# Kernel tuning notes

Measured on AMD Instinct MI355X. Metric: run time of the kernel, lower is better.

The kernel has to match this reference:

```python
import jax, jax.numpy as jnp
import numpy as np

B, C, H, W = 2, 128, 64, 64
EPS = 1e-5


def setup_inputs() -> dict:
    key = jax.random.key(0)
    ks = jax.random.split(key, 8)
    sc = 1.0 / np.sqrt(C)
    inp = {
        "x": jax.random.normal(ks[0], (B, C, H, W, 2), jnp.float32),
        # naive complex BN affine params: per-channel, per-component (real/imag)
        "bn_w": jnp.ones((C, 2), jnp.float32),
        "bn_b": jnp.zeros((C, 2), jnp.float32),
        # complex 1x1 conv weights: (out_c, in_c, 2) -> [..,0]=W_real, [..,1]=W_imag
        "wq": jax.random.normal(ks[1], (C, C, 2), jnp.float32) * sc,
        "bq": jnp.zeros((C, 2), jnp.float32),
        "wk": jax.random.normal(ks[2], (C, C, 2), jnp.float32) * sc,
        "bk": jnp.zeros((C, 2), jnp.float32),
        "wv": jax.random.normal(ks[3], (C, C, 2), jnp.float32) * sc,
        "bv": jnp.zeros((C, 2), jnp.float32),
        "gamma": jnp.float32(0.05),
    }
    return inp


def _complex_bn(x, w, b):
    # naive complex BN: normalize real and imag independently per channel
    # x: (B,C,H,W,2); stats over (B,H,W) per (C, component)
    mean = x.mean(axis=(0, 2, 3), keepdims=True)
    var = x.var(axis=(0, 2, 3), keepdims=True)
    xn = (x - mean) * jax.lax.rsqrt(var + EPS)
    return xn * w[None, :, None, None, :] + b[None, :, None, None, :]


def _complex_conv1x1(x, w, b):
    # x: (B,C,H,W,2); w: (O,C,2); b: (O,2)
    xr, xi = x[..., 0], x[..., 1]
    wr, wi = w[..., 0], w[..., 1]
    yr = jnp.einsum('oc,bchw->bohw', wr, xr) - jnp.einsum('oc,bchw->bohw', wi, xi)
    yi = jnp.einsum('oc,bchw->bohw', wr, xi) + jnp.einsum('oc,bchw->bohw', wi, xr)
    yr = yr + b[:, 0][None, :, None, None]
    yi = yi + b[:, 1][None, :, None, None]
    return jnp.stack([yr, yi], axis=-1)


def _attention(x, wq, bq, wk, bk, wv, bv, gamma):
    scale = C ** (-0.5)
    N = H * W
    # q,k,v: (B,C,H,W,2) -> (B,C,N,2) -> (B,N,C,2)
    to_tokens = lambda t: t.reshape(B, C, N, 2).transpose(0, 2, 1, 3)
    q = to_tokens(_complex_conv1x1(x, wq, bq))
    k = to_tokens(_complex_conv1x1(x, wk, bk))
    v = to_tokens(_complex_conv1x1(x, wv, bv))

    qr, qi = q[..., 0], q[..., 1]          # (B,N,C)
    kr, ki = k[..., 0], -k[..., 1]         # conjugate of k
    # k_t = conj(k) with token/channel axes swapped -> (B,C,N)
    ktr = kr.transpose(0, 2, 1)
    kti = ki.transpose(0, 2, 1)

    # complex matmul q @ k_t -> only the real part is used downstream
    attn_real = jnp.einsum('bnc,bcm->bnm', qr, ktr) - jnp.einsum('bnc,bcm->bnm', qi, kti)
    attn_w = jax.nn.softmax(attn_real * scale, axis=-1)  # (B,N,N)
    # dropout = identity (eval mode)

    # attn is purely real -> complex matmul reduces to two real matmuls
    out_r = jnp.einsum('bnm,bmc->bnc', attn_w, v[..., 0])
    out_i = jnp.einsum('bnm,bmc->bnc', attn_w, v[..., 1])
    out = jnp.stack([out_r, out_i], axis=-1)              # (B,N,C,2)
    out = out.transpose(0, 2, 1, 3).reshape(B, C, H, W, 2)
    return x + gamma * out


def reference(x, bn_w, bn_b, wq, bq, wk, bk, wv, bv, gamma):
    xn = _complex_bn(x, bn_w, bn_b)
    return _attention(xn, wq, bq, wk, bk, wv, bv, gamma)
```

## Files before the change

### kernel.cpp

```cpp
#include <hip/hip_runtime.h>
#include <hip/hip_bf16.h>

typedef __bf16 bf16_t;
typedef __bf16 bf16x8 __attribute__((ext_vector_type(8)));
typedef float  f32x4  __attribute__((ext_vector_type(4)));

#define MFMA16(A,B,C) __builtin_amdgcn_mfma_f32_16x16x32_bf16((A),(B),(C),0,0,0)

constexpr int Bn = 2, Cc = 128, Hh = 64, Wd = 64;
constexpr int N  = Hh * Wd;
constexpr int T  = Bn * N;
constexpr int D  = 2 * Cc;
constexpr int NSP = 8;
constexpr float EPS = 1e-5f;
constexpr float SCL = 0.08838834764831845f * 1.4426950408889634f;

__device__ __forceinline__ int tfrag(int row, int ch) {
    return (((ch >> 5) * 4 + (row >> 4)) << 10) +
           ((((ch >> 3) & 3) * 16 + (row & 15)) << 4) + (ch & 7) * 2;
}
__device__ __forceinline__ int vfrag(int ch, int key) {
    return (((key >> 5) * 16 + (ch >> 4)) << 10) +
           ((((key >> 3) & 3) * 16 + (ch & 15)) << 4) + (key & 7) * 2;
}

__device__ __forceinline__ void gl16(const void* g, void* l) {
    __builtin_amdgcn_global_load_lds(
        (const __attribute__((address_space(1))) void*)g,
        (__attribute__((address_space(3))) void*)l, 16, 0, 0);
}

__global__ void k_pre(const float* __restrict__ x, float4* __restrict__ part,
                      const float* __restrict__ wq, const float* __restrict__ wk,
                      const float* __restrict__ wv, const float* __restrict__ bq,
                      const float* __restrict__ bk, const float* __restrict__ bv,
                      char* __restrict__ Wg, float* __restrict__ bt) {
    int tid = threadIdx.x;
    if (blockIdx.x < 512) {
        int bid = blockIdx.x;
        int q = bid >> 7, c = bid & 127;
        float sr = 0.f, si = 0.f, qr = 0.f, qi = 0.f;
        for (int b = 0; b < Bn; ++b) {
            const float2* p = (const float2*)x + (size_t)(b * Cc + c) * N + q * 1024;
            for (int i = tid; i < 1024; i += 256) {
                float2 v = p[i];
                sr += v.x; si += v.y; qr += v.x * v.x; qi += v.y * v.y;
            }
        }
        #pragma unroll
        for (int d = 32; d >= 1; d >>= 1) {
            sr += __shfl_xor(sr, d); si += __shfl_xor(si, d);
            qr += __shfl_xor(qr, d); qi += __shfl_xor(qi, d);
        }
        __shared__ float red[4][4];
        int w = tid >> 6;
        if ((tid & 63) == 0) { red[w][0] = sr; red[w][1] = si; red[w][2] = qr; red[w][3] = qi; }
        __syncthreads();
        if (tid == 0) {
            part[c * 4 + q] = make_float4(red[0][0] + red[1][0] + red[2][0] + red[3][0],
                                          red[0][1] + red[1][1] + red[2][1] + red[3][1],
                                          red[0][2] + red[1][2] + red[2][2] + red[3][2],
                                          red[0][3] + red[1][3] + red[2][3] + red[3][3]);
        }
    } else {
        int o = blockIdx.x - 512;
        int k = tid;
        int proj = o >> 8, oc = o & 255;
        const float* wsrc = proj == 0 ? wq : (proj == 1 ? wk : wv);
        const float* bsrc = proj == 0 ? bq : (proj == 1 ? bk : bv);
        int co = oc >> 7, oo = oc & 127;
        int c = k & 127, kc = k >> 7;
        float val;
        if (co == 0) val = (kc == 0) ? wsrc[(oo * 128 + c) * 2 + 0] : -wsrc[(oo * 128 + c) * 2 + 1];
        else         val = (kc == 0) ? wsrc[(oo * 128 + c) * 2 + 1] :  wsrc[(oo * 128 + c) * 2 + 0];
        int tile = o >> 6, row = o & 63;
        *(bf16_t*)(Wg + (size_t)tile * 32768 + tfrag(row, k)) = (bf16_t)val;
        if (k == 0) bt[o] = bsrc[oo * 2 + co];
    }
}

__global__ void k_norm(const float* __restrict__ x, const float4* __restrict__ part,
                       const float* __restrict__ bn_w, const float* __restrict__ bn_b,
                       char* __restrict__ XNg) {
    __shared__ float4 ssl[128];
    __shared__ __align__(16) char Tsh[32768];
    int blk = blockIdx.x;
    int b = blk >> 6, hw0 = (blk & 63) * 64;
    int tid = threadIdx.x;
    if (tid < 128) {
        float4 p0 = part[tid * 4 + 0], p1 = part[tid * 4 + 1];
        float4 p2 = part[tid * 4 + 2], p3 = part[tid * 4 + 3];
        float sr = p0.x + p1.x + p2.x + p3.x, si = p0.y + p1.y + p2.y + p3.y;
        float qr = p0.z + p1.z + p2.z + p3.z, qi = p0.w + p1.w + p2.w + p3.w;
        const float inv = 1.0f / (float)(Bn * N);
        float mr = sr * inv, mi = si * inv;
        float vr = qr * inv - mr * mr, vi = qi * inv - mi * mi;
        float scr = bn_w[tid * 2 + 0] * rsqrtf(vr + EPS);
        float sci = bn_w[tid * 2 + 1] * rsqrtf(vi + EPS);
        ssl[tid] = make_float4(scr, bn_b[tid * 2 + 0] - mr * scr,
                               sci, bn_b[tid * 2 + 1] - mi * sci);
    }
    __syncthreads();
    const float2* xin = (const float2*)x;
    #pragma unroll
    for (int it = 0; it < 32; ++it) {
        int idx = it * 256 + tid;
        int c = idx >> 6, hw = idx & 63;
        size_t gi = (size_t)(b * Cc + c) * N + hw0 + hw;
        float2 v = xin[gi];
        float4 s = ssl[c];
        *(bf16_t*)(Tsh + tfrag(hw, c))       = (bf16_t)(v.x * s.x + s.y);
        *(bf16_t*)(Tsh + tfrag(hw, c + 128)) = (bf16_t)(v.y * s.z + s.w);
    }
    __syncthreads();
    #pragma unroll
    for (int it = 0; it < 8; ++it) {
        int idx = it * 256 + tid;
        *(uint4*)(XNg + (size_t)blk * 32768 + idx * 16) = *(const uint4*)(Tsh + idx * 16);
    }
}

__global__ __launch_bounds__(256) void k_qkv(const char* __restrict__ XNg,
        const char* __restrict__ Wg, const float* __restrict__ bt,
        char* __restrict__ Qg, char* __restrict__ Kg, char* __restrict__ Vg) {
    __shared__ __align__(16) char Xsh[32768];
    __shared__ __align__(16) char Wsh[32768];
    int mx = blockIdx.x, ny = blockIdx.y;
    int tid = threadIdx.x;
    int w = tid >> 6, lane = tid & 63, n15 = lane & 15, quad = lane >> 4;
    const char* xs = XNg + (size_t)mx * 32768;
    const char* wsp = Wg + (size_t)ny * 32768;
    #pragma unroll
    for (int i = 0; i < 8; ++i) {
        int off = (w * 8 + i) * 1024 + lane * 16;
        gl16(xs + off, Xsh + off);
        gl16(wsp + off, Wsh + off);
    }
    __syncthreads();
    f32x4 acc[4] = {};
    #pragma unroll
    for (int ks = 0; ks < 8; ++ks) {
        bf16x8 a = *(const bf16x8*)(Xsh + (ks * 4 + w) * 1024 + lane * 16);
        #pragma unroll
        for (int t = 0; t < 4; ++t) {
            bf16x8 bw = *(const bf16x8*)(Wsh + (ks * 4 + t) * 1024 + lane * 16);
            acc[t] = MFMA16(a, bw, acc[t]);
        }
    }
    int proj = ny >> 2;
    int jb = (ny & 3) * 64;
    #pragma unroll
    for (int t = 0; t < 4; ++t) {
        int j = jb + t * 16 + n15;
        float bias = bt[ny * 64 + t * 16 + n15];
        #pragma unroll
        for (int r = 0; r < 4; ++r) {
            int tk = mx * 64 + w * 16 + quad * 4 + r;
            float v = acc[t][r] + bias;
            int bb = tk >> 12, n = tk & (N - 1);
            if (proj == 0) {
                *(bf16_t*)(Qg + (size_t)(tk >> 6) * 32768 + tfrag(tk & 63, j)) = (bf16_t)v;
            } else {
                size_t tb = (size_t)(bb * 64 + (n >> 6)) * 32768;
                if (proj == 1) *(bf16_t*)(Kg + tb + tfrag(n & 63, j)) = (bf16_t)v;
                else           *(bf16_t*)(Vg + tb + vfrag(j, n & 63)) = (bf16_t)v;
            }
        }
    }
}

__global__ __launch_bounds__(256) void k_attn(const char* __restrict__ Qg,
        const char* __restrict__ Kg, const char* __restrict__ Vg,
        bf16_t* __restrict__ Opb, float* __restrict__ Lp) {
    __shared__ __align__(16) char Ksh[2 * 16384];
    __shared__ __align__(16) char Psh[4096];
    int bid = blockIdx.x;
    int grp = bid & 15, qt = bid >> 4;
    int sp = grp & 7, b = grp >> 3;
    int tid = threadIdx.x;
    int w = tid >> 6, lane = tid & 63, n15 = lane & 15, quad = lane >> 4;
    int r = w >> 1, h = w & 1;

    bf16x8 onef;
    #pragma unroll
    for (int i = 0; i < 8; ++i) onef[i] = (bf16_t)1.0f;

    bf16x8 qf[2][8];
    const char* qb = Qg + (size_t)(b * 64 + qt) * 32768;
    #pragma unroll
    for (int g = 0; g < 2; ++g)
        #pragma unroll
        for (int ks = 0; ks < 8; ++ks)
            qf[g][ks] = *(const bf16x8*)(qb + (ks * 4 + r * 2 + g) * 1024 + lane * 16);

    size_t kbase = (size_t)(b * 64 + sp * 8) * 32768;
    #pragma unroll
    for (int i = 0; i < 4; ++i) {
        int lf = w * 4 + i;
        gl16(Kg + kbase + (((lf >> 1) * 4 + (lf & 1)) << 10) + lane * 16,
             Ksh + (lf << 10) + lane * 16);
    }

    f32x4 o[4][4] = {};
    f32x4 l_[4] = {};

    for (int kt = 0; kt < 16; ++kt) {
        int cur = kt & 1;
        asm volatile("s_waitcnt vmcnt(0)" ::: "memory");
        __builtin_amdgcn_s_barrier();
        __builtin_amdgcn_sched_barrier(0);

        bf16x8 vf[4];
        const char* vt = Vg + kbase + (size_t)(kt >> 1) * 32768 + (kt & 1) * 16384;
        #pragma unroll
        for (int ct = 0; ct < 4; ++ct)
            vf[ct] = *(const bf16x8*)(vt + ((w * 4 + ct) << 10) + lane * 16);
        __builtin_amdgcn_sched_barrier(0);

        if (kt < 15) {
            int ck = kt + 1;
            char* kb = Ksh + (cur ^ 1) * 16384;
            #pragma unroll
            for (int i = 0; i < 4; ++i) {
                int lf = w * 4 + i;
                gl16(Kg + kbase + (size_t)(ck >> 1) * 32768 +
                         (((lf >> 1) * 4 + (ck & 1) * 2 + (lf & 1)) << 10) + lane * 16,
                     kb + (lf << 10) + lane * 16);
            }
        }

        const char* kc = Ksh + cur * 16384;
        f32x4 s0 = {}, s1 = {};
        __builtin_amdgcn_s_setprio(1);
        #pragma unroll
        for (int ks = 0; ks < 8; ++ks) {
            bf16x8 kf = *(const bf16x8*)(kc + ((ks * 2 + h) << 10) + lane * 16);
            s0 = MFMA16(qf[0][ks], kf, s0);
            s1 = MFMA16(qf[1][ks], kf, s1);
        }
        __builtin_amdgcn_s_setprio(0);

        #pragma unroll
        for (int ri = 0; ri < 4; ++ri) {
            float p0 = __builtin_amdgcn_exp2f(s0[ri] * SCL);
            float p1 = __builtin_amdgcn_exp2f(s1[ri] * SCL);
            int base = ((h * 2 + (n15 >> 3)) * 16 + quad * 4 + ri) * 16 + (n15 & 7) * 2;
            *(bf16_t*)(Psh + ((r * 2 + 0) << 10) + base) = (bf16_t)p0;
            *(bf16_t*)(Psh + ((r * 2 + 1) << 10) + base) = (bf16_t)p1;
        }
        asm volatile("s_waitcnt lgkmcnt(0)" ::: "memory");
        __builtin_amdgcn_s_barrier();
        __builtin_amdgcn_sched_barrier(0);

        bf16x8 pa[4];
        #pragma unroll
        for (int rf = 0; rf < 4; ++rf)
            pa[rf] = *(const bf16x8*)(Psh + (rf << 10) + lane * 16);
        __builtin_amdgcn_s_setprio(1);
        if (w == 0) {
            #pragma unroll
            for (int rf = 0; rf < 4; ++rf)
                l_[rf] = MFMA16(pa[rf], onef, l_[rf]);
        }
        #pragma unroll
        for (int rf = 0; rf < 4; ++rf)
            #pragma unroll
            for (int ct = 0; ct < 4; ++ct)
                o[rf][ct] = MFMA16(pa[rf], vf[ct], o[rf][ct]);
        __builtin_amdgcn_s_setprio(0);
    }
    int tok0 = b * N + qt * 64;
    #pragma unroll
    for (int rf = 0; rf < 4; ++rf)
        #pragma unroll
        for (int ct = 0; ct < 4; ++ct)
            #pragma unroll
            for (int ri = 0; ri < 4; ++ri)
                Opb[((size_t)sp * T + tok0 + rf * 16 + quad * 4 + ri) * D +
                    w * 64 + ct * 16 + n15] = (bf16_t)o[rf][ct][ri];
    if (w == 0 && n15 == 0) {
        #pragma unroll
        for (int rf = 0; rf < 4; ++rf)
            #pragma unroll
            for (int ri = 0; ri < 4; ++ri)
                Lp[sp * T + tok0 + rf * 16 + quad * 4 + ri] = l_[rf][ri];
    }
}

__global__ void k_comb(const bf16_t* __restrict__ Opb, const float* __restrict__ Lp,
                       const float4* __restrict__ part, const float* __restrict__ bn_w,
                       const float* __restrict__ bn_b, const float* __restrict__ x,
                       const float* __restrict__ gamma, float* __restrict__ out) {
    __shared__ float4 ssl[128];
    __shared__ float wts[32];
    __shared__ float Ot[256 * 33];
    int blk = blockIdx.x;
    int b = blk >> 7, hw0 = (blk & 127) * 32;
    int tok0 = b * N + hw0;
    int tid = threadIdx.x;
    if (tid < 128) {
        float4 p0 = part[tid * 4 + 0], p1 = part[tid * 4 + 1];
        float4 p2 = part[tid * 4 + 2], p3 = part[tid * 4 + 3];
        float sr = p0.x + p1.x + p2.x + p3.x, si = p0.y + p1.y + p2.y + p3.y;
        float qr = p0.z + p1.z + p2.z + p3.z, qi = p0.w + p1.w + p2.w + p3.w;
        const float inv = 1.0f / (float)(Bn * N);
        float mr = sr * inv, mi = si * inv;
        float vr = qr * inv - mr * mr, vi = qi * inv - mi * mi;
        float scr = bn_w[tid * 2 + 0] * rsqrtf(vr + EPS);
        float sci = bn_w[tid * 2 + 1] * rsqrtf(vi + EPS);
        ssl[tid] = make_float4(scr, bn_b[tid * 2 + 0] - mr * scr,
                               sci, bn_b[tid * 2 + 1] - mi * sci);
    }
    if (tid < 32) {
        float Z = 0.f;
        #pragma unroll
        for (int s = 0; s < NSP; ++s) Z += Lp[s * T + tok0 + tid];
        wts[tid] = gamma[0] / Z;
    }
    __syncthreads();
    #pragma unroll
    for (int i = 0; i < 4; ++i) {
        int idx = i * 256 + tid;
        int tk = idx >> 5, chunk = idx & 31;
        size_t base = (size_t)(tok0 + tk) * D + chunk * 8;
        float acc[8] = {};
        #pragma unroll
        for (int s = 0; s < NSP; ++s) {
            bf16x8 v = *(const bf16x8*)(Opb + (size_t)s * T * D + base);
            #pragma unroll
            for (int j = 0; j < 8; ++j) acc[j] += (float)v[j];
        }
        float ww = wts[tk];
        #pragma unroll
        for (int j = 0; j < 8; ++j) Ot[(chunk * 8 + j) * 33 + tk] = acc[j] * ww;
    }
    __syncthreads();
    const float2* xin = (const float2*)x;
    float2* xo = (float2*)out;
    #pragma unroll
    for (int i = 0; i < 16; ++i) {
        int linear = i * 256 + tid;
        int c = linear >> 5, hwo = linear & 31;
        size_t idx = (size_t)(b * Cc + c) * N + hw0 + hwo;
        float2 v = xin[idx];
        float4 s = ssl[c];
        float2 res;
        res.x = v.x * s.x + s.y + Ot[c * 33 + hwo];
        res.y = v.y * s.z + s.w + Ot[(128 + c) * 33 + hwo];
        xo[idx] = res;
    }
}

extern "C" void kernel_launch(void* const* d_in, const int* in_sizes, int n_in,
                              void* d_out, int out_size, void* d_ws, size_t ws_size,
                              hipStream_t stream) {
    const float* x    = (const float*)d_in[0];
    const float* bn_w = (const float*)d_in[1];
    const float* bn_b = (const float*)d_in[2];
    const float* wq   = (const float*)d_in[3];
    const float* bq   = (const float*)d_in[4];
    const float* wk   = (const float*)d_in[5];
    const float* bk   = (const float*)d_in[6];
    const float* wv   = (const float*)d_in[7];
    const float* bv   = (const float*)d_in[8];
    const float* gam  = (const float*)d_in[9];
    float* out = (float*)d_out;

    char* ws = (char*)d_ws;
    size_t off = 0;
    auto alloc = [&](size_t bytes) -> void* {
        void* p = ws + off;
        off += (bytes + 255) & ~(size_t)255;
        return p;
    };
    float4* part = (float4*)alloc(512 * sizeof(float4));
    char*   XNg  = (char*)alloc((size_t)128 * 32768);
    char*   Wg   = (char*)alloc((size_t)12 * 32768);
    float*  bt   = (float*)alloc(768 * 4);
    char*   Qg   = (char*)alloc((size_t)128 * 32768);
    char*   Kg   = (char*)alloc((size_t)128 * 32768);
    char*   Vg   = (char*)alloc((size_t)128 * 32768);
    bf16_t* Opb  = (bf16_t*)alloc((size_t)NSP * T * D * 2);
    float*  Lp   = (float*)alloc((size_t)NSP * T * 4);

    k_pre<<<1280, 256, 0, stream>>>(x, part, wq, wk, wv, bq, bk, bv, Wg, bt);
    k_norm<<<128, 256, 0, stream>>>(x, part, bn_w, bn_b, XNg);
    k_qkv<<<dim3(128, 12), 256, 0, stream>>>(XNg, Wg, bt, Qg, Kg, Vg);
    k_attn<<<1024, 256, 0, stream>>>(Qg, Kg, Vg, Opb, Lp);
    k_comb<<<256, 256, 0, stream>>>(Opb, Lp, part, bn_w, bn_b, x, gam, out);
}
```

Before: 160.1 us.

## Shrink attention query tile to 32, halve key splits, stage V through LDS

The attention kernel now handles 32 query rows per block instead of 64 and splits the keys 4 ways instead of 8, so each block loops over 32 key tiles. V tiles are loaded into LDS with global_load_lds together with K, which replaces direct global-to-register loads. K is no longer double-buffered: each iteration loads K and V synchronously between __syncthreads. Lower register and LDS use with launch_bounds(256,4) aims for higher occupancy and fewer partial results to combine, but it gives up the K prefetch overlap and halves MFMA reuse of each K/V fragment.

```diff
diff --git a/kernel.cpp b/kernel.cpp
--- a/kernel.cpp
+++ b/kernel.cpp
@@ -11,7 +11,7 @@
 constexpr int N  = Hh * Wd;
 constexpr int T  = Bn * N;
 constexpr int D  = 2 * Cc;
-constexpr int NSP = 8;
+constexpr int NSP = 4;
 constexpr float EPS = 1e-5f;
 constexpr float SCL = 0.08838834764831845f * 1.4426950408889634f;
 
@@ -169,14 +169,15 @@
     }
 }
 
-__global__ __launch_bounds__(256) void k_attn(const char* __restrict__ Qg,
+__global__ __launch_bounds__(256, 4) void k_attn(const char* __restrict__ Qg,
         const char* __restrict__ Kg, const char* __restrict__ Vg,
         bf16_t* __restrict__ Opb, float* __restrict__ Lp) {
-    __shared__ __align__(16) char Ksh[2 * 16384];
-    __shared__ __align__(16) char Psh[4096];
+    __shared__ __align__(16) char Ksh[16384];
+    __shared__ __align__(16) char Vsh[16384];
+    __shared__ __align__(16) char Psh[2048];
     int bid = blockIdx.x;
-    int grp = bid & 15, qt = bid >> 4;
-    int sp = grp & 7, b = grp >> 3;
+    int grp = bid & 7, qt = bid >> 3;
+    int sp = grp & 3, b = grp >> 2;
     int tid = threadIdx.x;
     int w = tid >> 6, lane = tid & 63, n15 = lane & 15, quad = lane >> 4;
     int r = w >> 1, h = w & 1;
@@ -185,93 +186,75 @@
     #pragma unroll
     for (int i = 0; i < 8; ++i) onef[i] = (bf16_t)1.0f;
 
-    bf16x8 qf[2][8];
-    const char* qb = Qg + (size_t)(b * 64 + qt) * 32768;
-    #pragma unroll
-    for (int g = 0; g < 2; ++g)
-        #pragma unroll
-        for (int ks = 0; ks < 8; ++ks)
-            qf[g][ks] = *(const bf16x8*)(qb + (ks * 4 + r * 2 + g) * 1024 + lane * 16);
-
-    size_t kbase = (size_t)(b * 64 + sp * 8) * 32768;
-    #pragma unroll
-    for (int i = 0; i < 4; ++i) {
-        int lf = w * 4 + i;
-        gl16(Kg + kbase + (((lf >> 1) * 4 + (lf & 1)) << 10) + lane * 16,
-             Ksh + (lf << 10) + lane * 16);
-    }
-
-    f32x4 o[4][4] = {};
-    f32x4 l_[4] = {};
-
-    for (int kt = 0; kt < 16; ++kt) {
-        int cur = kt & 1;
-        asm volatile("s_waitcnt vmcnt(0)" ::: "memory");
-        __builtin_amdgcn_s_barrier();
-        __builtin_amdgcn_sched_barrier(0);
-
-        bf16x8 vf[4];
-        const char* vt = Vg + kbase + (size_t)(kt >> 1) * 32768 + (kt & 1) * 16384;
-        #pragma unroll
-        for (int ct = 0; ct < 4; ++ct)
-            vf[ct] = *(const bf16x8*)(vt + ((w * 4 + ct) << 10) + lane * 16);
-        __builtin_amdgcn_sched_barrier(0);
-
-        if (kt < 15) {
-            int ck = kt + 1;
-            char* kb = Ksh + (cur ^ 1) * 16384;
-            #pragma unroll
-            for (int i = 0; i < 4; ++i) {
-                int lf = w * 4 + i;
-                gl16(Kg + kbase + (size_t)(ck >> 1) * 32768 +
-                         (((lf >> 1) * 4 + (ck & 1) * 2 + (lf & 1)) << 10) + lane * 16,
-                     kb + (lf << 10) + lane * 16);
-            }
-        }
-
-        const char* kc = Ksh + cur * 16384;
-        f32x4 s0 = {}, s1 = {};
+    bf16x8 qf[8];
+    const char* qb = Qg + (size_t)(b * 64 + (qt >> 1)) * 32768;
+    int qrow = (qt & 1) * 2 + r;
+    #pragma unroll
+    for (int ks = 0; ks < 8; ++ks)
+        qf[ks] = *(const bf16x8*)(qb + ((ks * 4 + qrow) << 10) + lane * 16);
+
+    size_t kbase = (size_t)(b * 64 + sp * 16) * 32768;
+
+    f32x4 o[2][4] = {};
+    f32x4 l_[2] = {};
+
+    #pragma unroll 2
+    for (int kt = 0; kt < 32; ++kt) {
+        __syncthreads();
+
+        const char* kg = Kg + kbase + (size_t)(kt >> 1) * 32768;
+        const char* vg = Vg + kbase + (size_t)(kt >> 1) * 32768 + (size_t)(kt & 1) * 16384;
+        #pragma unroll
+        for (int i = 0; i < 4; ++i) {
+            int lf = w * 4 + i;
+            gl16(kg + (((lf >> 1) * 4 + (kt & 1) * 2 + (lf & 1)) << 10) + lane * 16,
+                 Ksh + (lf << 10) + lane * 16);
+            gl16(vg + ((w * 4 + i) << 10) + lane * 16,
+                 Vsh + ((w * 4 + i) << 10) + lane * 16);
+        }
+        __syncthreads();
+
+        f32x4 s0 = {};
         __builtin_amdgcn_s_setprio(1);
         #pragma unroll
         for (int ks = 0; ks < 8; ++ks) {
-            bf16x8 kf = *(const bf16x8*)(kc + ((ks * 2 + h) << 10) + lane * 16);
-            s0 = MFMA16(qf[0][ks], kf, s0);
-            s1 = MFMA16(qf[1][ks], kf, s1);
+            bf16x8 kf = *(const bf16x8*)(Ksh + ((ks * 2 + h) << 10) + lane * 16);
+            s0 = MFMA16(qf[ks], kf, s0);
         }
         __builtin_amdgcn_s_setprio(0);
 
         #pragma unroll
         for (int ri = 0; ri < 4; ++ri) {
             float p0 = __builtin_amdgcn_exp2f(s0[ri] * SCL);
-            float p1 = __builtin_amdgcn_exp2f(s1[ri] * SCL);
             int base = ((h * 2 + (n15 >> 3)) * 16 + quad * 4 + ri) * 16 + (n15 & 7) * 2;
-            *(bf16_t*)(Psh + ((r * 2 + 0) << 10) + base) = (bf16_t)p0;
-            *(bf16_t*)(Psh + ((r * 2 + 1) << 10) + base) = (bf16_t)p1;
-        }
-        asm volatile("s_waitcnt lgkmcnt(0)" ::: "memory");
-        __builtin_amdgcn_s_barrier();
-        __builtin_amdgcn_sched_barrier(0);
-
-        bf16x8 pa[4];
-        #pragma unroll
-        for (int rf = 0; rf < 4; ++rf)
+            *(bf16_t*)(Psh + (r << 10) + base) = (bf16_t)p0;
+        }
+        __syncthreads();
+
+        bf16x8 pa[2];
+        #pragma unroll
+        for (int rf = 0; rf < 2; ++rf)
             pa[rf] = *(const bf16x8*)(Psh + (rf << 10) + lane * 16);
+        bf16x8 vf[4];
+        #pragma unroll
+        for (int ct = 0; ct < 4; ++ct)
+            vf[ct] = *(const bf16x8*)(Vsh + ((w * 4 + ct) << 10) + lane * 16);
         __builtin_amdgcn_s_setprio(1);
         if (w == 0) {
             #pragma unroll
-            for (int rf = 0; rf < 4; ++rf)
+            for (int rf = 0; rf < 2; ++rf)
                 l_[rf] = MFMA16(pa[rf], onef, l_[rf]);
         }
         #pragma unroll
-        for (int rf = 0; rf < 4; ++rf)
+        for (int rf = 0; rf < 2; ++rf)
             #pragma unroll
             for (int ct = 0; ct < 4; ++ct)
                 o[rf][ct] = MFMA16(pa[rf], vf[ct], o[rf][ct]);
         __builtin_amdgcn_s_setprio(0);
     }
-    int tok0 = b * N + qt * 64;
-    #pragma unroll
-    for (int rf = 0; rf < 4; ++rf)
+    int tok0 = b * N + qt * 32;
+    #pragma unroll
+    for (int rf = 0; rf < 2; ++rf)
         #pragma unroll
         for (int ct = 0; ct < 4; ++ct)
             #pragma unroll
@@ -280,7 +263,7 @@
                     w * 64 + ct * 16 + n15] = (bf16_t)o[rf][ct][ri];
     if (w == 0 && n15 == 0) {
         #pragma unroll
-        for (int rf = 0; rf < 4; ++rf)
+        for (int rf = 0; rf < 2; ++rf)
             #pragma unroll
             for (int ri = 0; ri < 4; ++ri)
                 Lp[sp * T + tok0 + rf * 16 + quad * 4 + ri] = l_[rf][ri];
```

After: 161.8 us. Within noise of the previous version (+1.1%).
